# Kernel tuning notes

Measured on AMD Instinct MI355X. Metric: run time of the kernel, lower is better.

Reference implementation:

```python
import jax, jax.numpy as jnp
import numpy as np
from jax import lax

EMBED = 512
HIDDEN = 1024
VOCAB = 50257
BATCH = 64


def setup_inputs() -> dict:
    key = jax.random.key(0)
    ks = jax.random.split(key, 7)
    s_ih = 1.0 / np.sqrt(HIDDEN)
    inp = {
        "features": jax.random.normal(ks[0], (BATCH, EMBED), dtype=jnp.float32),
        "W_ih": jax.random.uniform(ks[1], (4 * HIDDEN, EMBED), jnp.float32, -s_ih, s_ih),
        "W_hh": jax.random.uniform(ks[2], (4 * HIDDEN, HIDDEN), jnp.float32, -s_ih, s_ih),
        "b_ih": jax.random.uniform(ks[3], (4 * HIDDEN,), jnp.float32, -s_ih, s_ih),
        "b_hh": jax.random.uniform(ks[4], (4 * HIDDEN,), jnp.float32, -s_ih, s_ih),
        "W_fc": jax.random.uniform(ks[5], (VOCAB, HIDDEN), jnp.float32, -s_ih, s_ih),
        "b_fc": jax.random.uniform(ks[6], (VOCAB,), jnp.float32, -s_ih, s_ih),
        "max_seq_len": 18,
    }
    return inp


def reference(features, W_ih, W_hh, b_ih, b_hh, W_fc, b_fc, max_seq_len):
    # features: [B, E] fed at EVERY step (module re-feeds the same features).
    B = features.shape[0]
    H = W_hh.shape[1]
    # Input projection is constant across steps; hoist it (same math).
    x_proj = features @ W_ih.T + b_ih  # [B, 4H]

    def step(carry, _):
        h, c = carry
        gates = x_proj + h @ W_hh.T + b_hh  # [B, 4H], PyTorch gate order i,f,g,o
        i, f, g, o = jnp.split(gates, 4, axis=1)
        i = jax.nn.sigmoid(i)
        f = jax.nn.sigmoid(f)
        g = jnp.tanh(g)
        o = jax.nn.sigmoid(o)
        c_new = f * c + i * g
        h_new = o * jnp.tanh(c_new)
        out = h_new @ W_fc.T + b_fc  # [B, V]
        return (h_new, c_new), out

    h0 = jnp.zeros((B, H), dtype=features.dtype)
    c0 = jnp.zeros((B, H), dtype=features.dtype)
    _, outs = lax.scan(step, (h0, c0), None, length=max_seq_len)  # [T, B, V]
    return jnp.transpose(outs, (1, 0, 2))  # [B, T, V]
```

## Files before the change

kernel.cpp:

```cpp
#include <hip/hip_runtime.h>

#define EMBED  512
#define HIDDEN 1024
#define G4     4096
#define VOCAB  50257
#define BATCH  64
#define TSTEPS 18
#define MROWS  (BATCH*TSTEPS)

typedef __bf16 bf16x8 __attribute__((ext_vector_type(8)));
typedef float  f32x4  __attribute__((ext_vector_type(4)));

#define WS_HA_B   0
#define WS_HB_B   131072
#define WS_BAR_B  262144
#define WS_XB_B   524288
#define WS_HS_B   1572864

#define NLSTM_BLK 64

__device__ inline bf16x8 cvt2bf8(float4 a, float4 b) {
    bf16x8 v;
    v[0] = (__bf16)a.x; v[1] = (__bf16)a.y; v[2] = (__bf16)a.z; v[3] = (__bf16)a.w;
    v[4] = (__bf16)b.x; v[5] = (__bf16)b.y; v[6] = (__bf16)b.z; v[7] = (__bf16)b.w;
    return v;
}

__global__ __launch_bounds__(256) void k_xproj(const float* __restrict__ feat,
                                               const float* __restrict__ W_ih,
                                               const float* __restrict__ b_ih,
                                               const float* __restrict__ b_hh,
                                               float* __restrict__ xb,
                                               unsigned* __restrict__ bar) {
    if (blockIdx.x == 0 && blockIdx.y == 0 && threadIdx.x < 2)
        bar[threadIdx.x] = 0u;
    __shared__ float fsh[16][EMBED];
    const int tx = threadIdx.x;
    const int rc = blockIdx.x;
    const int b0 = blockIdx.y * 16;
    {
        int row = tx >> 4, seg = tx & 15;
        const float4* src = (const float4*)(feat + (b0 + row) * EMBED + seg * 32);
        float4* dst = (float4*)(&fsh[row][seg * 32]);
        #pragma unroll
        for (int c = 0; c < 8; ++c) dst[c] = src[c];
    }
    __syncthreads();
    const int jl = tx & 15, bl = tx >> 4;
    const int r = rc * 16 + jl;
    const int b = b0 + bl;
    const float4* w  = (const float4*)(W_ih + (size_t)r * EMBED);
    const float4* h4 = (const float4*)(&fsh[bl][0]);
    float acc = 0.f;
    #pragma unroll 4
    for (int k = 0; k < EMBED / 4; ++k) {
        float4 wv = w[k], hv = h4[k];
        acc += wv.x * hv.x + wv.y * hv.y + wv.z * hv.z + wv.w * hv.w;
    }
    xb[b * G4 + r] = acc + b_ih[r] + b_hh[r];
}

__device__ __forceinline__ void grid_barrier(unsigned* bar) {
    __syncthreads();
    if (threadIdx.x == 0) {
        __threadfence();
        unsigned gen = __hip_atomic_load(&bar[1], __ATOMIC_RELAXED, __HIP_MEMORY_SCOPE_AGENT);
        unsigned n = __hip_atomic_fetch_add(&bar[0], 1u, __ATOMIC_ACQ_REL, __HIP_MEMORY_SCOPE_AGENT);
        if (n == NLSTM_BLK - 1u) {
            __hip_atomic_store(&bar[0], 0u, __ATOMIC_RELAXED, __HIP_MEMORY_SCOPE_AGENT);
            __hip_atomic_store(&bar[1], gen + 1u, __ATOMIC_RELEASE, __HIP_MEMORY_SCOPE_AGENT);
        } else {
            while (__hip_atomic_load(&bar[1], __ATOMIC_ACQUIRE, __HIP_MEMORY_SCOPE_AGENT) == gen)
                __builtin_amdgcn_s_sleep(8);
        }
        __threadfence();
    }
    __syncthreads();
}

#define PJT 17

__global__ __launch_bounds__(256, 1) void k_lstm(const float* __restrict__ xb,
                                                 const float* __restrict__ Whh32,
                                                 __bf16* __restrict__ hA,
                                                 __bf16* __restrict__ hB,
                                                 __bf16* __restrict__ hs,
                                                 unsigned* __restrict__ bar) {
    __shared__ float part[16 * 64 * PJT];
    const int tx   = threadIdx.x;
    const int wave = tx >> 6;
    const int lane = tx & 63;
    const int q    = lane >> 4;
    const int r    = lane & 15;
    const int j0   = blockIdx.x * 16;
    const int kb   = wave * 256;

    bf16x8 bB[4][8];
    {
        const float* bsrc = Whh32 + (size_t)(j0 + r) * HIDDEN + kb + q * 8;
        #pragma unroll
        for (int g = 0; g < 4; ++g)
            #pragma unroll
            for (int s = 0; s < 8; ++s) {
                const float4* p = (const float4*)(bsrc + (size_t)g * 1024 * HIDDEN + s * 32);
                bB[g][s] = cvt2bf8(p[0], p[1]);
            }
    }

    const int jl = tx & 15;
    const int m0 = tx >> 4;
    float cr[4];
    float xbr[4][4];
    #pragma unroll
    for (int mi = 0; mi < 4; ++mi) {
        cr[mi] = 0.f;
        const int m = mi * 16 + m0;
        #pragma unroll
        for (int g = 0; g < 4; ++g)
            xbr[mi][g] = xb[m * G4 + g * 1024 + j0 + jl];
    }

    #pragma unroll
    for (int mi = 0; mi < 4; ++mi) {
        const int m = mi * 16 + m0;
        const float i_ = 1.f / (1.f + expf(-xbr[mi][0]));
        const float g_ = tanhf(xbr[mi][2]);
        const float o_ = 1.f / (1.f + expf(-xbr[mi][3]));
        const float cn = i_ * g_;
        cr[mi] = cn;
        const float hn = o_ * tanhf(cn);
        const __bf16 hb = (__bf16)hn;
        hB[m * HIDDEN + j0 + jl] = hb;
        hs[(size_t)(m * TSTEPS + 0) * HIDDEN + j0 + jl] = hb;
    }

    #pragma unroll 1
    for (int t = 1; t < TSTEPS; ++t) {
        grid_barrier(bar);
        const __bf16* hi = (t & 1) ? hB : hA;
        __bf16*       ho = (t & 1) ? hA : hB;

        f32x4 acc[4][4];
        #pragma unroll
        for (int i = 0; i < 4; ++i)
            #pragma unroll
            for (int g = 0; g < 4; ++g)
                acc[i][g] = (f32x4){0.f, 0.f, 0.f, 0.f};

        const __bf16* aBase = hi + (size_t)r * HIDDEN + kb + q * 8;
        #pragma unroll
        for (int s = 0; s < 8; ++s) {
            const int ko = s * 32;
            bf16x8 av[4];
            #pragma unroll
            for (int i = 0; i < 4; ++i)
                av[i] = *(const bf16x8*)(aBase + (size_t)i * 16 * HIDDEN + ko);
            #pragma unroll
            for (int i = 0; i < 4; ++i)
                #pragma unroll
                for (int g = 0; g < 4; ++g)
                    acc[i][g] = __builtin_amdgcn_mfma_f32_16x16x32_bf16(av[i], bB[g][s], acc[i][g], 0, 0, 0);
        }

        #pragma unroll
        for (int i = 0; i < 4; ++i)
            #pragma unroll
            for (int g = 0; g < 4; ++g)
                #pragma unroll
                for (int reg = 0; reg < 4; ++reg)
                    part[((wave * 4 + g) * 64 + i * 16 + q * 4 + reg) * PJT + r] = acc[i][g][reg];
        __syncthreads();

        #pragma unroll
        for (int mi = 0; mi < 4; ++mi) {
            const int m = mi * 16 + m0;
            float gsum[4];
            #pragma unroll
            for (int g = 0; g < 4; ++g) {
                float s = xbr[mi][g];
                #pragma unroll
                for (int w = 0; w < 4; ++w)
                    s += part[((w * 4 + g) * 64 + m) * PJT + jl];
                gsum[g] = s;
            }
            const float i_ = 1.f / (1.f + expf(-gsum[0]));
            const float f_ = 1.f / (1.f + expf(-gsum[1]));
            const float g_ = tanhf(gsum[2]);
            const float o_ = 1.f / (1.f + expf(-gsum[3]));
            const float cn = f_ * cr[mi] + i_ * g_;
            cr[mi] = cn;
            const float hn = o_ * tanhf(cn);
            const __bf16 hb = (__bf16)hn;
            ho[m * HIDDEN + j0 + jl] = hb;
            hs[(size_t)(m * TSTEPS + t) * HIDDEN + j0 + jl] = hb;
        }
    }
}

#define LPITCH 40
#define NBLK 393
#define MBLK 9
#define NWG  (NBLK*MBLK)
#define XQ   (NWG/8)
#define XR   (NWG%8)

__global__ __launch_bounds__(256) void k_fc(const __bf16* __restrict__ hs,
                                            const float* __restrict__ W_fc,
                                            const float* __restrict__ b_fc,
                                            float* __restrict__ out) {
    __shared__ __bf16 Ash[128 * LPITCH];
    __shared__ __bf16 Bsh[128 * LPITCH];
    const int tx = threadIdx.x;
    const int bid = blockIdx.x;
    const int xcd = bid & 7;
    const int lid = bid >> 3;
    const int base = (xcd < XR) ? xcd * (XQ + 1) : XR * (XQ + 1) + (xcd - XR) * XQ;
    const int virt = base + lid;
    const int mb = (virt % MBLK) * 128;
    const int nb = (virt / MBLK) * 128;

    const int srow = tx >> 1;
    const int half = tx & 1;
    const __bf16* aSrc = hs + (size_t)(mb + srow) * HIDDEN + half * 16;
    const int nclamp = min(nb + srow, VOCAB - 1);
    const float4* bSrc = (const float4*)(W_fc + (size_t)nclamp * HIDDEN + half * 16);
    __bf16* aDst = &Ash[srow * LPITCH + half * 16];
    __bf16* bDst = &Bsh[srow * LPITCH + half * 16];

    const int lane = tx & 63;
    const int wave = tx >> 6;
    const int q = lane >> 4;
    const int r = lane & 15;
    const int wm = (wave >> 1) * 64;
    const int wn = (wave & 1) * 64;

    const __bf16* aF[4];
    const __bf16* bF[4];
    #pragma unroll
    for (int i = 0; i < 4; ++i) aF[i] = &Ash[(wm + i * 16 + r) * LPITCH + q * 8];
    #pragma unroll
    for (int j = 0; j < 4; ++j) bF[j] = &Bsh[(wn + j * 16 + r) * LPITCH + q * 8];

    f32x4 acc[4][4];
    #pragma unroll
    for (int i = 0; i < 4; ++i)
        #pragma unroll
        for (int j = 0; j < 4; ++j)
            acc[i][j] = (f32x4){0.f, 0.f, 0.f, 0.f};

    bf16x8 a0p = *(const bf16x8*)aSrc;
    bf16x8 a1p = *(const bf16x8*)(aSrc + 8);
    float4 f0p = bSrc[0], f1p = bSrc[1], f2p = bSrc[2], f3p = bSrc[3];
    aSrc += 32; bSrc += 8;

    for (int k0 = 0; k0 < HIDDEN; k0 += 32) {
        *(bf16x8*)aDst = a0p;
        *(bf16x8*)(aDst + 8) = a1p;
        *(bf16x8*)bDst = cvt2bf8(f0p, f1p);
        *(bf16x8*)(bDst + 8) = cvt2bf8(f2p, f3p);
        __syncthreads();
        if (k0 + 32 < HIDDEN) {
            a0p = *(const bf16x8*)aSrc;
            a1p = *(const bf16x8*)(aSrc + 8);
            f0p = bSrc[0]; f1p = bSrc[1]; f2p = bSrc[2]; f3p = bSrc[3];
            aSrc += 32; bSrc += 8;
        }
        bf16x8 av[4], bv[4];
        #pragma unroll
        for (int i = 0; i < 4; ++i) av[i] = *(const bf16x8*)aF[i];
        #pragma unroll
        for (int j = 0; j < 4; ++j) bv[j] = *(const bf16x8*)bF[j];
        #pragma unroll
        for (int i = 0; i < 4; ++i)
            #pragma unroll
            for (int j = 0; j < 4; ++j)
                acc[i][j] = __builtin_amdgcn_mfma_f32_16x16x32_bf16(av[i], bv[j], acc[i][j], 0, 0, 0);
        __syncthreads();
    }

    #pragma unroll
    for (int j = 0; j < 4; ++j) {
        const int v = nb + wn + j * 16 + r;
        if (v < VOCAB) {
            const float bias = b_fc[v];
            #pragma unroll
            for (int i = 0; i < 4; ++i) {
                const int m0 = mb + wm + i * 16 + q * 4;
                float* op = out + (size_t)m0 * VOCAB + v;
                op[0]                 = acc[i][j][0] + bias;
                op[(size_t)VOCAB]     = acc[i][j][1] + bias;
                op[(size_t)VOCAB * 2] = acc[i][j][2] + bias;
                op[(size_t)VOCAB * 3] = acc[i][j][3] + bias;
            }
        }
    }
}

extern "C" void kernel_launch(void* const* d_in, const int* in_sizes, int n_in,
                              void* d_out, int out_size, void* d_ws, size_t ws_size,
                              hipStream_t stream) {
    const float* feat = (const float*)d_in[0];
    const float* W_ih = (const float*)d_in[1];
    const float* W_hh = (const float*)d_in[2];
    const float* b_ih = (const float*)d_in[3];
    const float* b_hh = (const float*)d_in[4];
    const float* W_fc = (const float*)d_in[5];
    const float* b_fc = (const float*)d_in[6];
    float* out = (float*)d_out;

    char* wsb = (char*)d_ws;
    __bf16*   hA  = (__bf16*)(wsb + WS_HA_B);
    __bf16*   hB  = (__bf16*)(wsb + WS_HB_B);
    unsigned* bar = (unsigned*)(wsb + WS_BAR_B);
    float*    xb  = (float*)(wsb + WS_XB_B);
    __bf16*   hs  = (__bf16*)(wsb + WS_HS_B);

    k_xproj<<<dim3(256, 4), 256, 0, stream>>>(feat, W_ih, b_ih, b_hh, xb, bar);
    k_lstm<<<NLSTM_BLK, 256, 0, stream>>>(xb, W_hh, hA, hB, hs, bar);
    k_fc<<<NWG, 256, 0, stream>>>(hs, W_fc, b_fc, out);
}
```

Baseline: 929.7 us.

## Replace atomic grid barrier with per-block step flags and pipeline h loads

```diff
diff --git a/kernel.cpp b/kernel.cpp
--- a/kernel.cpp
+++ b/kernel.cpp
@@ -31,9 +31,11 @@
                                                const float* __restrict__ b_ih,
                                                const float* __restrict__ b_hh,
                                                float* __restrict__ xb,
-                                               unsigned* __restrict__ bar) {
-    if (blockIdx.x == 0 && blockIdx.y == 0 && threadIdx.x < 2)
-        bar[threadIdx.x] = 0u;
+                                               unsigned* __restrict__ flags) {
+    if (blockIdx.x == 0 && blockIdx.y == 0) {
+        #pragma unroll
+        for (int k = 0; k < 8; ++k) flags[threadIdx.x * 8 + k] = 0u;
+    }
     __shared__ float fsh[16][EMBED];
     const int tx = threadIdx.x;
     const int rc = blockIdx.x;
@@ -60,39 +62,71 @@
     xb[b * G4 + r] = acc + b_ih[r] + b_hh[r];
 }
 
-__device__ __forceinline__ void grid_barrier(unsigned* bar) {
+__device__ __forceinline__ void store_h_sc(__bf16* p, __bf16 v) {
+    unsigned hv = (unsigned)__builtin_bit_cast(unsigned short, v);
+    asm volatile("global_store_short %0, %1, off sc0 sc1" :: "v"(p), "v"(hv) : "memory");
+}
+
+#define WAIT0 asm volatile("s_waitcnt vmcnt(0)" ::: "memory")
+#define WAIT4 asm volatile("s_waitcnt vmcnt(4)" ::: "memory")
+#define SBAR  __builtin_amdgcn_sched_barrier(0)
+
+__device__ __forceinline__ void step_barrier(unsigned* flags, int bid, int wave,
+                                             int lane, unsigned t) {
+    WAIT0;
     __syncthreads();
     if (threadIdx.x == 0) {
-        __threadfence();
-        unsigned gen = __hip_atomic_load(&bar[1], __ATOMIC_RELAXED, __HIP_MEMORY_SCOPE_AGENT);
-        unsigned n = __hip_atomic_fetch_add(&bar[0], 1u, __ATOMIC_ACQ_REL, __HIP_MEMORY_SCOPE_AGENT);
-        if (n == NLSTM_BLK - 1u) {
-            __hip_atomic_store(&bar[0], 0u, __ATOMIC_RELAXED, __HIP_MEMORY_SCOPE_AGENT);
-            __hip_atomic_store(&bar[1], gen + 1u, __ATOMIC_RELEASE, __HIP_MEMORY_SCOPE_AGENT);
-        } else {
-            while (__hip_atomic_load(&bar[1], __ATOMIC_ACQUIRE, __HIP_MEMORY_SCOPE_AGENT) == gen)
-                __builtin_amdgcn_s_sleep(8);
+        unsigned* fp = flags + (size_t)bid * 32;
+        asm volatile("global_store_dword %0, %1, off sc0 sc1" :: "v"(fp), "v"(t) : "memory");
+    }
+    if (wave == 0) {
+        const unsigned* pp = flags + (size_t)lane * 32;
+        unsigned v;
+        for (;;) {
+            asm volatile("global_load_dword %0, %1, off sc0 sc1\n\t"
+                         "s_waitcnt vmcnt(0)"
+                         : "=&v"(v) : "v"(pp) : "memory");
+            if (__all((int)(v >= t))) break;
+            __builtin_amdgcn_s_sleep(1);
         }
-        __threadfence();
     }
     __syncthreads();
 }
 
 #define PJT 17
+
+#define LOADS(dst, sidx) do {                                                   \
+    const int _ko = (sidx) * 32;                                                \
+    _Pragma("unroll")                                                           \
+    for (int _i = 0; _i < 4; ++_i) {                                            \
+        const __bf16* _p = aBase + (size_t)_i * 16 * HIDDEN + _ko;              \
+        asm volatile("global_load_dwordx4 %0, %1, off sc0 sc1"                  \
+                     : "=&v"(dst[_i]) : "v"(_p) : "memory");                    \
+    } } while (0)
+
+#define MFMAS(src, sidx) do {                                                   \
+    _Pragma("unroll")                                                           \
+    for (int _i = 0; _i < 4; ++_i)                                              \
+        _Pragma("unroll")                                                       \
+        for (int _g = 0; _g < 4; ++_g)                                          \
+            acc[_i][_g] = __builtin_amdgcn_mfma_f32_16x16x32_bf16(              \
+                src[_i], bB[_g][sidx], acc[_i][_g], 0, 0, 0);                   \
+    } while (0)
 
 __global__ __launch_bounds__(256, 1) void k_lstm(const float* __restrict__ xb,
                                                  const float* __restrict__ Whh32,
                                                  __bf16* __restrict__ hA,
                                                  __bf16* __restrict__ hB,
                                                  __bf16* __restrict__ hs,
-                                                 unsigned* __restrict__ bar) {
+                                                 unsigned* __restrict__ flags) {
     __shared__ float part[16 * 64 * PJT];
     const int tx   = threadIdx.x;
     const int wave = tx >> 6;
     const int lane = tx & 63;
     const int q    = lane >> 4;
     const int r    = lane & 15;
-    const int j0   = blockIdx.x * 16;
+    const int bid  = blockIdx.x;
+    const int j0   = bid * 16;
     const int kb   = wave * 256;
 
     bf16x8 bB[4][8];
@@ -130,13 +164,13 @@
         cr[mi] = cn;
         const float hn = o_ * tanhf(cn);
         const __bf16 hb = (__bf16)hn;
-        hB[m * HIDDEN + j0 + jl] = hb;
+        store_h_sc(hB + m * HIDDEN + j0 + jl, hb);
         hs[(size_t)(m * TSTEPS + 0) * HIDDEN + j0 + jl] = hb;
     }
 
     #pragma unroll 1
     for (int t = 1; t < TSTEPS; ++t) {
-        grid_barrier(bar);
+        step_barrier(flags, bid, wave, lane, (unsigned)t);
         const __bf16* hi = (t & 1) ? hB : hA;
         __bf16*       ho = (t & 1) ? hA : hB;
 
@@ -148,19 +182,24 @@
                 acc[i][g] = (f32x4){0.f, 0.f, 0.f, 0.f};
 
         const __bf16* aBase = hi + (size_t)r * HIDDEN + kb + q * 8;
-        #pragma unroll
-        for (int s = 0; s < 8; ++s) {
-            const int ko = s * 32;
-            bf16x8 av[4];
-            #pragma unroll
-            for (int i = 0; i < 4; ++i)
-                av[i] = *(const bf16x8*)(aBase + (size_t)i * 16 * HIDDEN + ko);
-            #pragma unroll
-            for (int i = 0; i < 4; ++i)
-                #pragma unroll
-                for (int g = 0; g < 4; ++g)
-                    acc[i][g] = __builtin_amdgcn_mfma_f32_16x16x32_bf16(av[i], bB[g][s], acc[i][g], 0, 0, 0);
-        }
+        bf16x8 avA[4], avB[4];
+
+        LOADS(avA, 0);
+        LOADS(avB, 1);
+        WAIT4; SBAR; MFMAS(avA, 0);
+        LOADS(avA, 2);
+        WAIT4; SBAR; MFMAS(avB, 1);
+        LOADS(avB, 3);
+        WAIT4; SBAR; MFMAS(avA, 2);
+        LOADS(avA, 4);
+        WAIT4; SBAR; MFMAS(avB, 3);
+        LOADS(avB, 5);
+        WAIT4; SBAR; MFMAS(avA, 4);
+        LOADS(avA, 6);
+        WAIT4; SBAR; MFMAS(avB, 5);
+        LOADS(avB, 7);
+        WAIT4; SBAR; MFMAS(avA, 6);
+        WAIT0; SBAR; MFMAS(avB, 7);
 
         #pragma unroll
         for (int i = 0; i < 4; ++i)
@@ -191,9 +230,10 @@
             cr[mi] = cn;
             const float hn = o_ * tanhf(cn);
             const __bf16 hb = (__bf16)hn;
-            ho[m * HIDDEN + j0 + jl] = hb;
+            store_h_sc(ho + m * HIDDEN + j0 + jl, hb);
             hs[(size_t)(m * TSTEPS + t) * HIDDEN + j0 + jl] = hb;
         }
+        __syncthreads();
     }
 }
 
@@ -309,13 +349,13 @@
     float* out = (float*)d_out;
 
     char* wsb = (char*)d_ws;
-    __bf16*   hA  = (__bf16*)(wsb + WS_HA_B);
-    __bf16*   hB  = (__bf16*)(wsb + WS_HB_B);
-    unsigned* bar = (unsigned*)(wsb + WS_BAR_B);
-    float*    xb  = (float*)(wsb + WS_XB_B);
-    __bf16*   hs  = (__bf16*)(wsb + WS_HS_B);
-
-    k_xproj<<<dim3(256, 4), 256, 0, stream>>>(feat, W_ih, b_ih, b_hh, xb, bar);
-    k_lstm<<<NLSTM_BLK, 256, 0, stream>>>(xb, W_hh, hA, hB, hs, bar);
+    __bf16*   hA    = (__bf16*)(wsb + WS_HA_B);
+    __bf16*   hB    = (__bf16*)(wsb + WS_HB_B);
+    unsigned* flags = (unsigned*)(wsb + WS_BAR_B);
+    float*    xb    = (float*)(wsb + WS_XB_B);
+    __bf16*   hs    = (__bf16*)(wsb + WS_HS_B);
+
+    k_xproj<<<dim3(256, 4), 256, 0, stream>>>(feat, W_ih, b_ih, b_hh, xb, flags);
+    k_lstm<<<NLSTM_BLK, 256, 0, stream>>>(xb, W_hh, hA, hB, hs, flags);
     k_fc<<<NWG, 256, 0, stream>>>(hs, W_fc, b_fc, out);
 }
```

After: 814.6 us. 12.4% less time.
